# Kernel optimization log

Hardware: AMD Instinct MI355X
Metric: run time of the kernel (lower is better)

Reference implementation:

```python
import jax, jax.numpy as jnp
import numpy as np

B = 1048576
K = 10  # max set size for presence/absent letter sets
D = 8   # letter_embedding_dim
H = 256 # mlp_hidden_dim
TOTAL = (5 + 5) * D + 2 * D  # 96


def setup_inputs() -> dict:
    key = jax.random.key(0)
    ks = jax.random.split(key, 12)
    return {
        "guess_indices": jax.random.randint(ks[0], (B, 5), 0, 26),
        "constraint_indices": jax.random.randint(ks[1], (B, 5), 0, 27),
        "presence_idx": jax.random.randint(ks[2], (B, K), 0, 26),
        "presence_len": jax.random.randint(ks[3], (B,), 0, K + 1),
        "absent_idx": jax.random.randint(ks[4], (B, K), 0, 26),
        "absent_len": jax.random.randint(ks[5], (B,), 0, K + 1),
        "guess_table": jax.random.normal(ks[6], (26, D), dtype=jnp.float32),
        "constraint_table": jax.random.normal(ks[7], (27, D), dtype=jnp.float32),
        "W1": jax.random.normal(ks[8], (TOTAL, H), dtype=jnp.float32) * 0.1,
        "b1": jnp.zeros((H,), dtype=jnp.float32),
        "W2": jax.random.normal(ks[9], (H, 1), dtype=jnp.float32) * 0.1,
        "b2": jnp.zeros((1,), dtype=jnp.float32),
    }


def _masked_mean(table, idx, ln):
    # Segment-mean over padded letter sets; empty set -> zeros (matches aggregate_set).
    emb = table[idx]  # [B, K, D]
    mask = (jnp.arange(idx.shape[1])[None, :] < ln[:, None]).astype(emb.dtype)  # [B, K]
    s = jnp.einsum('bkd,bk->bd', emb, mask)
    denom = jnp.maximum(ln, 1).astype(emb.dtype)[:, None]
    return jnp.where(ln[:, None] > 0, s / denom, jnp.zeros_like(s))


def reference(guess_indices, constraint_indices, presence_idx, presence_len,
              absent_idx, absent_len, guess_table, constraint_table,
              W1, b1, W2, b2):
    bsz = guess_indices.shape[0]
    guess_flat = guess_table[guess_indices].reshape(bsz, -1)            # [B, 5*D]
    constraint_flat = constraint_table[constraint_indices].reshape(bsz, -1)  # [B, 5*D]
    presence_agg = _masked_mean(guess_table, presence_idx, presence_len)     # [B, D]
    absent_agg = _masked_mean(guess_table, absent_idx, absent_len)           # [B, D]
    combined = jnp.concatenate([guess_flat, constraint_flat, presence_agg, absent_agg], axis=1)
    # MLP (dropout is identity in eval mode)
    h = jax.nn.relu(combined @ W1 + b1)
    return h @ W2 + b2  # [B, 1]
```

## Files before the change

kernel.cpp:

```cpp
#include <hip/hip_runtime.h>

typedef __attribute__((ext_vector_type(8))) short short8;
typedef __attribute__((ext_vector_type(16))) float f32x16;

#define WS_GT   0
#define WS_CT   256
#define WS_W1T  512

__device__ __forceinline__ unsigned short f2bf(float f) {
    unsigned int u = __float_as_uint(f);
    u = (u + 0x7fffu + ((u >> 16) & 1u)) >> 16;
    return (unsigned short)u;
}
__device__ __forceinline__ float bflo(unsigned int w) { return __uint_as_float(w << 16); }
__device__ __forceinline__ float bfhi(unsigned int w) { return __uint_as_float(w & 0xffff0000u); }

__global__ __launch_bounds__(256) void prep_kernel(
    const float* __restrict__ gt, const float* __restrict__ ct,
    const float* __restrict__ W1, const float* __restrict__ b1,
    unsigned short* __restrict__ ws)
{
    int tid = blockIdx.x * 256 + threadIdx.x;
    if (tid < 208) ws[WS_GT + tid] = f2bf(gt[tid]);
    if (tid < 216) ws[WS_CT + tid] = f2bf(ct[tid]);
    if (tid < 24576) {
        int kl  = tid >> 8;
        int col = tid & 255;
        int chunk = kl >> 3, j = kl & 7;
        int hi, kk;
        if (chunk < 5)        { hi = 0; kk = chunk; }
        else if (chunk < 10)  { hi = 1; kk = chunk - 5; }
        else if (chunk == 10) { hi = 0; kk = 5; }
        else                  { hi = 1; kk = 5; }
        int s = kk * 2 + hi;
        ws[WS_W1T + col * 104 + s * 8 + j] = f2bf(W1[kl * 256 + col]);
    } else if (tid < 26624) {
        int idx2 = tid - 24576;
        int col = idx2 >> 3, j = idx2 & 7;
        ws[WS_W1T + col * 104 + 96 + j] = (j == 0) ? f2bf(b1[col]) : (unsigned short)0;
    }
}

__global__ __launch_bounds__(256, 2) void wordle_kernel(
    const int* __restrict__ gidx, const int* __restrict__ cidx,
    const int* __restrict__ pidx, const int* __restrict__ plen,
    const int* __restrict__ aidx, const int* __restrict__ alen,
    const float* __restrict__ W2, const float* __restrict__ b2,
    const unsigned short* __restrict__ ws,
    float* __restrict__ out, int tilesPerBlock)
{
    __shared__ unsigned short w1t[26624];
    __shared__ float outbuf[128];

    {
        const uint4* src = (const uint4*)(ws + WS_W1T);
        uint4* dst = (uint4*)w1t;
        int tid = threadIdx.x;
        #pragma unroll
        for (int i = 0; i < 13; ++i) dst[tid + i * 256] = src[tid + i * 256];
    }
    __syncthreads();

    const int lane = threadIdx.x & 63;
    const int wv   = threadIdx.x >> 6;
    const int l31  = lane & 31;
    const int hi   = lane >> 5;
    const unsigned short* gt = ws + WS_GT;
    const unsigned short* ct = ws + WS_CT;
    const unsigned short* tb = hi ? ct : gt;
    const float b2v = b2[0];

    short8 a6 = {0, 0, 0, 0, 0, 0, 0, 0};
    a6[0] = hi ? (short)0 : (short)0x3F80;

    float w2r[8];
    #pragma unroll
    for (int nt = 0; nt < 8; ++nt) w2r[nt] = W2[nt * 32 + l31];

    int ip0, ip1, ip2, ip3, ip4;
    int s0, s1, s2, s3, s4, s5, s6, s7, s8, s9;
    int lenv;

#define LOADIDX(T) do {                                                     \
        const int r_ = (blockIdx.x * tilesPerBlock + (T)) * 128 + wv * 32 + l31; \
        const int* ip_ = (hi ? cidx : gidx) + r_ * 5;                       \
        ip0 = ip_[0]; ip1 = ip_[1]; ip2 = ip_[2]; ip3 = ip_[3]; ip4 = ip_[4]; \
        const int* si_ = (hi ? aidx : pidx) + r_ * 10;                      \
        s0 = si_[0]; s1 = si_[1]; s2 = si_[2]; s3 = si_[3]; s4 = si_[4];    \
        s5 = si_[5]; s6 = si_[6]; s7 = si_[7]; s8 = si_[8]; s9 = si_[9];    \
        lenv = (hi ? alen : plen)[r_];                                      \
    } while (0)

    LOADIDX(0);

    for (int t = 0; t < tilesPerBlock; ++t) {
        const int tile = blockIdx.x * tilesPerBlock + t;

        short8 a0 = *(const short8*)(tb + ip0 * 8);
        short8 a1 = *(const short8*)(tb + ip1 * 8);
        short8 a2 = *(const short8*)(tb + ip2 * 8);
        short8 a3 = *(const short8*)(tb + ip3 * 8);
        short8 a4 = *(const short8*)(tb + ip4 * 8);
        uint4 e0 = *(const uint4*)(gt + s0 * 8);
        uint4 e1 = *(const uint4*)(gt + s1 * 8);
        uint4 e2 = *(const uint4*)(gt + s2 * 8);
        uint4 e3 = *(const uint4*)(gt + s3 * 8);
        uint4 e4 = *(const uint4*)(gt + s4 * 8);
        uint4 e5 = *(const uint4*)(gt + s5 * 8);
        uint4 e6 = *(const uint4*)(gt + s6 * 8);
        uint4 e7 = *(const uint4*)(gt + s7 * 8);
        uint4 e8 = *(const uint4*)(gt + s8 * 8);
        uint4 e9 = *(const uint4*)(gt + s9 * 8);
        const int len = lenv;

        if (t + 1 < tilesPerBlock) LOADIDX(t + 1);

        short8 a5;
        {
            float m0=0.f,m1=0.f,m2=0.f,m3=0.f,m4=0.f,m5=0.f,m6=0.f,m7=0.f;
            uint4 ev[10] = {e0,e1,e2,e3,e4,e5,e6,e7,e8,e9};
            #pragma unroll
            for (int k = 0; k < 10; ++k) {
                float w = (k < len) ? 1.f : 0.f;
                m0 += w * bflo(ev[k].x); m1 += w * bfhi(ev[k].x);
                m2 += w * bflo(ev[k].y); m3 += w * bfhi(ev[k].y);
                m4 += w * bflo(ev[k].z); m5 += w * bfhi(ev[k].z);
                m6 += w * bflo(ev[k].w); m7 += w * bfhi(ev[k].w);
            }
            const float scl = (len > 0) ? (1.f / (float)len) : 0.f;
            a5[0] = (short)f2bf(m0 * scl); a5[1] = (short)f2bf(m1 * scl);
            a5[2] = (short)f2bf(m2 * scl); a5[3] = (short)f2bf(m3 * scl);
            a5[4] = (short)f2bf(m4 * scl); a5[5] = (short)f2bf(m5 * scl);
            a5[6] = (short)f2bf(m6 * scl); a5[7] = (short)f2bf(m7 * scl);
        }

        f32x16 acc[8];
        #pragma unroll
        for (int nt = 0; nt < 8; ++nt)
            #pragma unroll
            for (int r = 0; r < 16; ++r) acc[nt][r] = 0.f;

        #pragma unroll
        for (int nt = 0; nt < 8; ++nt) {
            const int col = nt * 32 + l31;
            short8 bv = *(const short8*)(&w1t[col * 104 + 96]);
            acc[nt] = __builtin_amdgcn_mfma_f32_32x32x16_bf16(a6, bv, acc[nt], 0, 0, 0);
        }
        #pragma unroll
        for (int kk = 0; kk < 6; ++kk) {
            const short8 av = (kk == 0) ? a0 : (kk == 1) ? a1 : (kk == 2) ? a2
                           : (kk == 3) ? a3 : (kk == 4) ? a4 : a5;
            const int s = kk * 2 + hi;
            #pragma unroll
            for (int nt = 0; nt < 8; ++nt) {
                const int col = nt * 32 + l31;
                short8 bv = *(const short8*)(&w1t[col * 104 + s * 8]);
                acc[nt] = __builtin_amdgcn_mfma_f32_32x32x16_bf16(av, bv, acc[nt], 0, 0, 0);
            }
        }

        float part[16];
        #pragma unroll
        for (int r = 0; r < 16; ++r) part[r] = 0.f;
        #pragma unroll
        for (int nt = 0; nt < 8; ++nt) {
            #pragma unroll
            for (int r = 0; r < 16; ++r) {
                float h = acc[nt][r];
                h = h > 0.f ? h : 0.f;
                part[r] += h * w2r[nt];
            }
        }

        const int b_ = (l31 >> 4) & 1, c_ = (l31 >> 3) & 1,
                  d_ = (l31 >> 2) & 1, e_ = (l31 >> 1) & 1;
        float p1[8], p2[4], p3[2], p4, p5;
        #pragma unroll
        for (int i = 0; i < 8; ++i) {
            float keep = b_ ? part[8 + i] : part[i];
            float send = b_ ? part[i]     : part[8 + i];
            p1[i] = keep + __shfl_xor(send, 16, 64);
        }
        #pragma unroll
        for (int i = 0; i < 4; ++i) {
            float keep = c_ ? p1[4 + i] : p1[i];
            float send = c_ ? p1[i]     : p1[4 + i];
            p2[i] = keep + __shfl_xor(send, 8, 64);
        }
        #pragma unroll
        for (int i = 0; i < 2; ++i) {
            float keep = d_ ? p2[2 + i] : p2[i];
            float send = d_ ? p2[i]     : p2[2 + i];
            p3[i] = keep + __shfl_xor(send, 4, 64);
        }
        {
            float keep = e_ ? p3[1] : p3[0];
            float send = e_ ? p3[0] : p3[1];
            p4 = keep + __shfl_xor(send, 2, 64);
        }
        p5 = p4 + __shfl_xor(p4, 1, 64);

        if (!(lane & 1)) {
            const int r = l31 >> 1;
            outbuf[wv * 32 + 4 * hi + (r & 3) + 8 * (r >> 2)] = p5 + b2v;
        }
        asm volatile("s_waitcnt lgkmcnt(0)" ::: "memory");
        if (lane < 32) {
            out[tile * 128 + wv * 32 + lane] = outbuf[wv * 32 + lane];
        }
    }
#undef LOADIDX
}

extern "C" void kernel_launch(void* const* d_in, const int* in_sizes, int n_in,
                              void* d_out, int out_size, void* d_ws, size_t ws_size,
                              hipStream_t stream) {
    const int*   gidx = (const int*)d_in[0];
    const int*   cidx = (const int*)d_in[1];
    const int*   pidx = (const int*)d_in[2];
    const int*   plen = (const int*)d_in[3];
    const int*   aidx = (const int*)d_in[4];
    const int*   alen = (const int*)d_in[5];
    const float* gt   = (const float*)d_in[6];
    const float* ct   = (const float*)d_in[7];
    const float* W1   = (const float*)d_in[8];
    const float* b1   = (const float*)d_in[9];
    const float* W2   = (const float*)d_in[10];
    const float* b2   = (const float*)d_in[11];
    float* out = (float*)d_out;
    unsigned short* ws = (unsigned short*)d_ws;

    const int B = in_sizes[0] / 5;
    prep_kernel<<<104, 256, 0, stream>>>(gt, ct, W1, b1, ws);

    const int tilesTotal = B / 128;
    int tpb = 16;
    while (tpb > 1 && (tilesTotal % tpb)) tpb >>= 1;
    const int blocks = tilesTotal / tpb;
    wordle_kernel<<<blocks, 256, 0, stream>>>(gidx, cidx, pidx, plen, aidx, alen,
                                              W2, b2, ws, out, tpb);
}
```

Baseline: 80.95 us.

## Split hidden columns across wave pairs and reorder MFMAs before set aggregation

Each pair of waves now handles the same 32 rows, and each wave computes only half of the 256 hidden columns. This halves the accumulator registers per wave and lets the two partial outputs be summed through double-buffered shared memory, at the cost of a block-wide barrier every tile. The MFMAs for the direct embedding slots are issued before the masked-mean computation so matrix work can overlap with the gather latency of the set embeddings. Tiles shrink to 64 rows with more tiles per block, and index and gather loads for a row are now duplicated across two waves.

```diff
diff --git a/kernel.cpp b/kernel.cpp
--- a/kernel.cpp
+++ b/kernel.cpp
@@ -50,7 +50,7 @@
     float* __restrict__ out, int tilesPerBlock)
 {
     __shared__ unsigned short w1t[26624];
-    __shared__ float outbuf[128];
+    __shared__ float outbuf[2][128];
 
     {
         const uint4* src = (const uint4*)(ws + WS_W1T);
@@ -63,6 +63,8 @@
 
     const int lane = threadIdx.x & 63;
     const int wv   = threadIdx.x >> 6;
+    const int rg   = wv >> 1;
+    const int ch   = wv & 1;
     const int l31  = lane & 31;
     const int hi   = lane >> 5;
     const unsigned short* gt = ws + WS_GT;
@@ -73,16 +75,16 @@
     short8 a6 = {0, 0, 0, 0, 0, 0, 0, 0};
     a6[0] = hi ? (short)0 : (short)0x3F80;
 
-    float w2r[8];
+    float w2r[4];
     #pragma unroll
-    for (int nt = 0; nt < 8; ++nt) w2r[nt] = W2[nt * 32 + l31];
+    for (int j = 0; j < 4; ++j) w2r[j] = W2[(ch * 4 + j) * 32 + l31];
 
     int ip0, ip1, ip2, ip3, ip4;
     int s0, s1, s2, s3, s4, s5, s6, s7, s8, s9;
     int lenv;
 
 #define LOADIDX(T) do {                                                     \
-        const int r_ = (blockIdx.x * tilesPerBlock + (T)) * 128 + wv * 32 + l31; \
+        const int r_ = (blockIdx.x * tilesPerBlock + (T)) * 64 + rg * 32 + l31; \
         const int* ip_ = (hi ? cidx : gidx) + r_ * 5;                       \
         ip0 = ip_[0]; ip1 = ip_[1]; ip2 = ip_[2]; ip3 = ip_[3]; ip4 = ip_[4]; \
         const int* si_ = (hi ? aidx : pidx) + r_ * 10;                      \
@@ -115,6 +117,31 @@
 
         if (t + 1 < tilesPerBlock) LOADIDX(t + 1);
 
+        f32x16 acc[4];
+        #pragma unroll
+        for (int j = 0; j < 4; ++j)
+            #pragma unroll
+            for (int r = 0; r < 16; ++r) acc[j][r] = 0.f;
+
+        #pragma unroll
+        for (int j = 0; j < 4; ++j) {
+            const int col = (ch * 4 + j) * 32 + l31;
+            short8 bv = *(const short8*)(&w1t[col * 104 + 96]);
+            acc[j] = __builtin_amdgcn_mfma_f32_32x32x16_bf16(a6, bv, acc[j], 0, 0, 0);
+        }
+        #pragma unroll
+        for (int kk = 0; kk < 5; ++kk) {
+            const short8 av = (kk == 0) ? a0 : (kk == 1) ? a1 : (kk == 2) ? a2
+                           : (kk == 3) ? a3 : a4;
+            const int s = kk * 2 + hi;
+            #pragma unroll
+            for (int j = 0; j < 4; ++j) {
+                const int col = (ch * 4 + j) * 32 + l31;
+                short8 bv = *(const short8*)(&w1t[col * 104 + s * 8]);
+                acc[j] = __builtin_amdgcn_mfma_f32_32x32x16_bf16(av, bv, acc[j], 0, 0, 0);
+            }
+        }
+
         short8 a5;
         {
             float m0=0.f,m1=0.f,m2=0.f,m3=0.f,m4=0.f,m5=0.f,m6=0.f,m7=0.f;
@@ -134,41 +161,23 @@
             a5[6] = (short)f2bf(m6 * scl); a5[7] = (short)f2bf(m7 * scl);
         }
 
-        f32x16 acc[8];
-        #pragma unroll
-        for (int nt = 0; nt < 8; ++nt)
-            #pragma unroll
-            for (int r = 0; r < 16; ++r) acc[nt][r] = 0.f;
-
-        #pragma unroll
-        for (int nt = 0; nt < 8; ++nt) {
-            const int col = nt * 32 + l31;
-            short8 bv = *(const short8*)(&w1t[col * 104 + 96]);
-            acc[nt] = __builtin_amdgcn_mfma_f32_32x32x16_bf16(a6, bv, acc[nt], 0, 0, 0);
-        }
-        #pragma unroll
-        for (int kk = 0; kk < 6; ++kk) {
-            const short8 av = (kk == 0) ? a0 : (kk == 1) ? a1 : (kk == 2) ? a2
-                           : (kk == 3) ? a3 : (kk == 4) ? a4 : a5;
-            const int s = kk * 2 + hi;
-            #pragma unroll
-            for (int nt = 0; nt < 8; ++nt) {
-                const int col = nt * 32 + l31;
-                short8 bv = *(const short8*)(&w1t[col * 104 + s * 8]);
-                acc[nt] = __builtin_amdgcn_mfma_f32_32x32x16_bf16(av, bv, acc[nt], 0, 0, 0);
-            }
+        #pragma unroll
+        for (int j = 0; j < 4; ++j) {
+            const int col = (ch * 4 + j) * 32 + l31;
+            short8 bv = *(const short8*)(&w1t[col * 104 + (10 + hi) * 8]);
+            acc[j] = __builtin_amdgcn_mfma_f32_32x32x16_bf16(a5, bv, acc[j], 0, 0, 0);
         }
 
         float part[16];
         #pragma unroll
         for (int r = 0; r < 16; ++r) part[r] = 0.f;
         #pragma unroll
-        for (int nt = 0; nt < 8; ++nt) {
+        for (int j = 0; j < 4; ++j) {
             #pragma unroll
             for (int r = 0; r < 16; ++r) {
-                float h = acc[nt][r];
+                float h = acc[j][r];
                 h = h > 0.f ? h : 0.f;
-                part[r] += h * w2r[nt];
+                part[r] += h * w2r[j];
             }
         }
 
@@ -202,11 +211,12 @@
 
         if (!(lane & 1)) {
             const int r = l31 >> 1;
-            outbuf[wv * 32 + 4 * hi + (r & 3) + 8 * (r >> 2)] = p5 + b2v;
-        }
-        asm volatile("s_waitcnt lgkmcnt(0)" ::: "memory");
-        if (lane < 32) {
-            out[tile * 128 + wv * 32 + lane] = outbuf[wv * 32 + lane];
+            outbuf[t & 1][ch * 64 + rg * 32 + 4 * hi + (r & 3) + 8 * (r >> 2)] = p5;
+        }
+        __syncthreads();
+        if (threadIdx.x < 64) {
+            out[tile * 64 + threadIdx.x] =
+                outbuf[t & 1][threadIdx.x] + outbuf[t & 1][64 + threadIdx.x] + b2v;
         }
     }
 #undef LOADIDX
@@ -233,8 +243,8 @@
     const int B = in_sizes[0] / 5;
     prep_kernel<<<104, 256, 0, stream>>>(gt, ct, W1, b1, ws);
 
-    const int tilesTotal = B / 128;
-    int tpb = 16;
+    const int tilesTotal = B / 64;
+    int tpb = 32;
     while (tpb > 1 && (tilesTotal % tpb)) tpb >>= 1;
     const int blocks = tilesTotal / tpb;
     wordle_kernel<<<blocks, 256, 0, stream>>>(gidx, cidx, pidx, plen, aidx, alen,
```

New measurement: 105.0 us. +29.8%, slower.
